# Kernel tuning notes

Hardware: AMD Instinct MI355X
Metric: run time of the kernel (lower is better)

## Reference

```python
import jax, jax.numpy as jnp
import numpy as np

N_WAY = 2
K_SHOT = 5
C = 320
NPTS = 2048
NQ = 2
K_PROTO = 100  # hardcoded k=100 in forward
N_CLS = N_WAY + 1
SIGMA = 1.0
NEG = -1e9


def _l2norm(x, eps=1e-8):
    return x / (jnp.linalg.norm(x, axis=-1, keepdims=True) + eps)


def _class_prototypes(feat, mask, k):
    """Multi-prototype masked pooling for one class.
    feat: [M, C] point features; mask: [M] float (1 = belongs to class).
    Picks k masked seed points, assigns every masked point to its
    nearest (cosine) seed, and returns the k masked cluster means.
    """
    M = feat.shape[0]
    # deterministic seeds: first k masked points (tie-break by index)
    score = mask - jnp.arange(M, dtype=feat.dtype) * 1e-9
    _, seed_idx = jax.lax.top_k(score, k)
    seeds = feat[seed_idx]                      # [k, C]
    sim = _l2norm(feat) @ _l2norm(seeds).T      # [M, k]
    assign = jnp.argmax(sim, axis=1)            # [M]
    onehot = jax.nn.one_hot(assign, k, dtype=feat.dtype) * mask[:, None]  # [M, k]
    num = onehot.T @ feat                       # [k, C]
    den = onehot.sum(axis=0)[:, None] + 1e-8
    return num / den


def _fg_prototypes(support_feat, fg_mask, k):
    # support_feat [n_way, k_shot, C, N] -> per-class point sets [n_way, k_shot*N, C]
    feat = support_feat.transpose(0, 1, 3, 2).reshape(N_WAY, -1, C)
    m = fg_mask.reshape(N_WAY, -1).astype(feat.dtype)
    protos = jax.vmap(lambda f, mm: _class_prototypes(f, mm, k))(feat, m)  # [n_way, k, C]
    labels = jnp.repeat(jnp.arange(1, N_WAY + 1), k)                        # classes 1..n_way
    return protos.reshape(-1, C), jax.nn.one_hot(labels, N_CLS, dtype=feat.dtype)


def _bg_prototypes(support_feat, bg_mask, k):
    feat = support_feat.transpose(0, 1, 3, 2).reshape(-1, C)   # all shots pooled
    m = bg_mask.reshape(-1).astype(feat.dtype)
    protos = _class_prototypes(feat, m, k)                      # [k, C]
    labels = jnp.zeros((k,), dtype=jnp.int32)                   # class 0 = background
    return protos, jax.nn.one_hot(labels, N_CLS, dtype=feat.dtype)


def _predict(prototypes, proto_onehot, qfeat, qlabels):
    # cosine similarity [M, P], per-class max over that class's prototypes
    sim = (_l2norm(qfeat) @ _l2norm(prototypes).T) / SIGMA        # [M, P]
    cls_mask = proto_onehot.T[None] > 0                            # [1, ncls, P]
    pred = jnp.max(jnp.where(cls_mask, sim[:, None, :], NEG), axis=-1)  # [M, ncls]
    logp = jax.nn.log_softmax(pred, axis=-1)
    loss = -jnp.mean(jnp.take_along_axis(logp, qlabels.reshape(-1, 1), axis=1))
    query_pred = pred.reshape(NQ, NPTS, N_CLS).transpose(0, 2, 1)  # [NQ, ncls, NPTS]
    return loss, query_pred


def reference(support_feat, query_feat, support_y, query_y):
    fg_mask = support_y
    bg_mask = 1 - support_y
    fg_protos, fg_labels = _fg_prototypes(support_feat, fg_mask, K_PROTO)
    bg_protos, bg_labels = _bg_prototypes(support_feat, bg_mask, K_PROTO)
    prototypes = jnp.concatenate([bg_protos, fg_protos], axis=0)           # [P, C]
    proto_labels = jnp.concatenate([bg_labels, fg_labels], axis=0)         # [P, ncls]

    qfeat = query_feat.transpose(0, 2, 1).reshape(-1, C)                   # [NQ*NPTS, C]
    loss, query_pred = _predict(prototypes, proto_labels, qfeat, query_y)
    # the forward adds computeCrossEntropyLoss(query_pred, query_y): same CE again
    loss = loss * 2.0

    # post-hoc per-point confidence thresholding (vectorized Python loop)
    qp = jnp.concatenate([query_pred[0], query_pred[1]], axis=-1)          # [ncls, NQ*NPTS]
    predictions = jnp.argmax(qp, axis=0)
    confidences = jnp.max(qp, axis=0)
    final = jnp.where(confidences > jnp.mean(confidences), predictions, -1)
    final_labels = jnp.stack([final[:NPTS], final[NPTS:]], axis=0)         # [2, NPTS]
    return loss, query_pred, final_labels


def setup_inputs() -> dict:
    key = jax.random.key(0)
    k1, k2, k3, k4 = jax.random.split(key, 4)
    return {
        "support_feat": jax.random.normal(k1, (N_WAY, K_SHOT, C, NPTS), dtype=jnp.float32),
        "query_feat": jax.random.normal(k2, (NQ, C, NPTS), dtype=jnp.float32),
        "support_y": jax.random.randint(k3, (N_WAY, K_SHOT, NPTS), 0, 2, dtype=jnp.int32),
        "query_y": jax.random.randint(k4, (NQ, NPTS), 0, 3, dtype=jnp.int32),
    }
```

## Files before the change

kernel.cpp:

```cpp
#include <hip/hip_runtime.h>
#include <math.h>

#define C 320
#define NPTS 2048
#define SUPPTS 20480
#define QPTS 4096
#define KP 100
#define NCLS 3
#define PSTRIDE 300

__global__ __launch_bounds__(64) void k_protoseed(const float* __restrict__ sup,
                                                  const int* __restrict__ sy,
                                                  float* __restrict__ pbP,
                                                  int* __restrict__ cntG) {
    int p    = blockIdx.x;
    int lane = threadIdx.x;
    if (lane == 0) cntG[p] = 0;
    int prob = (p < 100) ? 2 : ((p < 200) ? 0 : 1);
    int rank = (p < 100) ? p : ((p < 200) ? p - 100 : p - 200);
    int M    = (prob == 2) ? SUPPTS : 10240;
    int base = (prob == 1) ? 10240 : 0;
    int found = 0, sp = 0;
    for (int chunk = 0; chunk < M; chunk += 64) {
        int yy = sy[base + chunk + lane];
        int m  = (prob == 2) ? (1 - yy) : yy;
        unsigned long long bal = __ballot(m != 0);
        int cnt = __popcll(bal);
        if (found + cnt > rank) {
            int need = rank - found;
            int prefix = __popcll(bal & ((1ull << lane) - 1ull));
            unsigned long long match = __ballot(m && (prefix == need));
            int pos = __ffsll((unsigned long long)match) - 1;
            sp = base + chunk + pos;
            break;
        }
        found += cnt;
    }
    const float* fb = sup + ((size_t)(sp >> 11) * C) * NPTS + (sp & 2047);
    float v[5]; float s = 0.f;
    #pragma unroll
    for (int i = 0; i < 5; i++) {
        v[i] = fb[(size_t)(lane + i * 64) * NPTS];
        s += v[i] * v[i];
    }
    #pragma unroll
    for (int off = 32; off > 0; off >>= 1) s += __shfl_down(s, off);
    s = __shfl(s, 0);
    float r = 1.0f / (sqrtf(s) + 1e-8f);
    int tile, slot;
    if (p < 100)      { tile = p / 10;              slot = p % 10; }
    else if (p < 200) { tile = 10 + (p - 100) / 10; slot = (p - 100) % 10; }
    else              { tile = 20 + (p - 200) / 10; slot = (p - 200) % 10; }
    #pragma unroll
    for (int i = 0; i < 5; i++)
        pbP[(size_t)(lane + i * 64) * 480 + tile * 16 + slot] = v[i] * r;
}

__global__ __launch_bounds__(256) void k_assign(const float* __restrict__ sup,
                                                const float* __restrict__ pbP,
                                                float* __restrict__ pmaxv,
                                                int* __restrict__ pmaxj) {
    int b = blockIdx.x, jt = blockIdx.y, tid = threadIdx.x;
    int w = (b >= 40) ? 1 : 0;
    int g = b * 256 + tid;
    const float* fb = sup + ((size_t)(g >> 11) * C) * NPTS + (g & 2047);
    const float* rbb = pbP + (size_t)jt * 16;
    const float* rfb = pbP + (size_t)(10 + w * 10 + jt) * 16;
    float accB[10], accF[10];
    #pragma unroll
    for (int j = 0; j < 10; j++) { accB[j] = 0.f; accF[j] = 0.f; }
    float pf[8];
    #pragma unroll
    for (int k = 0; k < 8; k++) pf[k] = fb[(size_t)k * NPTS];
    for (int cc = 0; cc < C; cc += 8) {
        float cur[8];
        #pragma unroll
        for (int k = 0; k < 8; k++) cur[k] = pf[k];
        if (cc + 8 < C) {
            #pragma unroll
            for (int k = 0; k < 8; k++) pf[k] = fb[(size_t)(cc + 8 + k) * NPTS];
        }
        #pragma unroll
        for (int k = 0; k < 8; k++) {
            const float* rb = rbb + (size_t)(cc + k) * 480;
            const float* rf = rfb + (size_t)(cc + k) * 480;
            float px = cur[k];
            #pragma unroll
            for (int j = 0; j < 10; j++) {
                accB[j] += px * rb[j];
                accF[j] += px * rf[j];
            }
        }
    }
    float bvB = accB[0]; int bjB = 0;
    float bvF = accF[0]; int bjF = 0;
    #pragma unroll
    for (int j = 1; j < 10; j++) {
        if (accB[j] > bvB) { bvB = accB[j]; bjB = j; }
        if (accF[j] > bvF) { bvF = accF[j]; bjF = j; }
    }
    size_t a0 = (size_t)jt * 40960 + g;
    pmaxv[a0] = bvB;          pmaxj[a0] = jt * 10 + bjB;
    pmaxv[a0 + 20480] = bvF;  pmaxj[a0 + 20480] = jt * 10 + bjF;
}

__global__ __launch_bounds__(256) void k_combine_dst(const float* __restrict__ pmaxv,
                                                     const int* __restrict__ pmaxj,
                                                     const int* __restrict__ sy,
                                                     int* __restrict__ dst,
                                                     float* __restrict__ loss,
                                                     int* __restrict__ cntG) {
    int g = blockIdx.x * 256 + threadIdx.x;
    if (g == 0) loss[0] = 0.f;
    if (g == 1) loss[1] = 0.f;
    float bvB = pmaxv[g];         int bjB = pmaxj[g];
    float bvF = pmaxv[20480 + g]; int bjF = pmaxj[20480 + g];
    #pragma unroll
    for (int t = 1; t < 10; t++) {
        size_t base = (size_t)t * 40960;
        float vB = pmaxv[base + g];
        if (vB > bvB) { bvB = vB; bjB = pmaxj[base + g]; }
        float vF = pmaxv[base + 20480 + g];
        if (vF > bvF) { bvF = vF; bjF = pmaxj[base + 20480 + g]; }
    }
    int way = (g >= 10240) ? 1 : 0;
    int dv = sy[g] ? (100 + way * 100 + bjF) : bjB;
    dst[g] = dv;
    atomicAdd(&cntG[dv], 1);
}

__global__ __launch_bounds__(256) void k_accum_lds(const float* __restrict__ sup,
                                                   const int* __restrict__ dst,
                                                   float* __restrict__ part) {
    __shared__ float bins[4 * 200 * 16];
    __shared__ int   dl[1024];
    int bx = blockIdx.x;
    int by = blockIdx.y;
    int tid = threadIdx.x;
    int ws = bx >> 1, half = bx & 1;
    int wmask = (ws >= 5) ? 1 : 0;
    int c0 = by * 16;

    int4 d4 = *(const int4*)(dst + ws * 2048 + half * 1024 + 4 * tid);
    dl[4 * tid + 0] = (d4.x < 100) ? d4.x : (d4.x - wmask * 100);
    dl[4 * tid + 1] = (d4.y < 100) ? d4.y : (d4.y - wmask * 100);
    dl[4 * tid + 2] = (d4.z < 100) ? d4.z : (d4.z - wmask * 100);
    dl[4 * tid + 3] = (d4.w < 100) ? d4.w : (d4.w - wmask * 100);
    for (int i = tid; i < 4 * 200 * 16; i += 256) bins[i] = 0.f;
    __syncthreads();

    int wv = tid >> 6, lane = tid & 63;
    int ch = lane & 15, pq = lane >> 4;
    float* mybins = bins + wv * 3200;
    const int* dlp = dl + wv * 256 + pq;
    const float* fb = sup + ((size_t)(ws * C + c0 + ch)) * NPTS + half * 1024 + wv * 256 + pq;

    int   b_cur = dlp[0];
    float f_cur = fb[0];
    for (int it = 0; it < 64; it++) {
        int nidx = (it < 63) ? (it + 1) * 4 : 0;
        int   b_nxt = dlp[nidx];
        float f_nxt = fb[nidx];
        int b0 = __builtin_amdgcn_readlane(b_cur, 0);
        int b1 = __builtin_amdgcn_readlane(b_cur, 16);
        int b2 = __builtin_amdgcn_readlane(b_cur, 32);
        int b3 = __builtin_amdgcn_readlane(b_cur, 48);
        bool dup = (b0 == b1) | (b0 == b2) | (b0 == b3) |
                   (b1 == b2) | (b1 == b3) | (b2 == b3);
        int addr = b_cur * 16 + ch;
        if (!dup) {
            mybins[addr] += f_cur;
        } else {
            unsafeAtomicAdd(&mybins[addr], f_cur);
        }
        b_cur = b_nxt; f_cur = f_nxt;
    }
    __syncthreads();

    for (int i = tid; i < 3200; i += 256) {
        int bin = i >> 4, c = i & 15;
        float s = bins[bin * 16 + c] + bins[3200 + bin * 16 + c]
                + bins[6400 + bin * 16 + c] + bins[9600 + bin * 16 + c];
        int ct8 = by * 2 + (c >> 3);
        part[(size_t)(bx * 40 + ct8) * 1600 + bin * 8 + (c & 7)] = s;
    }
}

__global__ __launch_bounds__(64) void k_reduce_proto(const float* __restrict__ part,
                                                     const int* __restrict__ cntG,
                                                     float* __restrict__ phatT) {
    int d   = blockIdx.x;
    int tid = threadIdx.x;
    int local, s0, ns;
    if (d < 100)      { local = d;       s0 = 0;  ns = 20; }
    else if (d < 200) { local = d;       s0 = 0;  ns = 10; }
    else              { local = d - 100; s0 = 10; ns = 10; }
    float dn = (float)cntG[d];
    float inv = 1.0f / (dn + 1e-8f);
    float vals[5]; float sq = 0.f;
    #pragma unroll
    for (int i = 0; i < 5; i++) {
        int c = tid + i * 64;
        int ct = c >> 3, cl = c & 7;
        float s = 0.f;
        for (int k = 0; k < ns; k++)
            s += part[(size_t)((s0 + k) * 40 + ct) * 1600 + local * 8 + cl];
        float v = s * inv;
        vals[i] = v; sq += v * v;
    }
    #pragma unroll
    for (int off = 32; off > 0; off >>= 1) sq += __shfl_down(sq, off);
    sq = __shfl(sq, 0);
    float rn = 1.0f / (sqrtf(sq) + 1e-8f);
    #pragma unroll
    for (int i = 0; i < 5; i++)
        phatT[(size_t)(tid + i * 64) * PSTRIDE + d] = vals[i] * rn;
}

__global__ __launch_bounds__(256) void k_qpartial(const float* __restrict__ qry,
                                                  const float* __restrict__ phT,
                                                  float* __restrict__ qmaxv,
                                                  float* __restrict__ qrn) {
    __shared__ float shp[C * 16];
    __shared__ float red[3 * 64 * 45];
    int pb = blockIdx.x, jt = blockIdx.y, tid = threadIdx.x;
    int wave = tid >> 6, lane = tid & 63;
    int j0 = jt * 10;
    for (int i = tid; i < C * 10; i += 256) {
        int j = i % 10, c = i / 10;
        shp[c * 16 + j] = phT[(size_t)c * PSTRIDE + j0 + j];
    }
    __syncthreads();
    int m = pb * 256 + lane * 4;
    int c0 = wave * 80;
    const float* fb = qry + ((size_t)(m >> 11) * C + c0) * NPTS + (m & 2047);
    float acc[4][10];
    #pragma unroll
    for (int p = 0; p < 4; p++)
        #pragma unroll
        for (int j = 0; j < 10; j++) acc[p][j] = 0.f;
    float qn[4] = {0.f, 0.f, 0.f, 0.f};
    float4 pf[8];
    #pragma unroll
    for (int k = 0; k < 8; k++) pf[k] = *(const float4*)(fb + (size_t)k * NPTS);
    for (int cc = 0; cc < 80; cc += 8) {
        float4 cur[8];
        #pragma unroll
        for (int k = 0; k < 8; k++) cur[k] = pf[k];
        if (cc + 8 < 80) {
            #pragma unroll
            for (int k = 0; k < 8; k++) pf[k] = *(const float4*)(fb + (size_t)(cc + 8 + k) * NPTS);
        }
        #pragma unroll
        for (int k = 0; k < 8; k++) {
            const float* row = &shp[(c0 + cc + k) * 16];
            float4 p0 = ((const float4*)row)[0];
            float4 p1 = ((const float4*)row)[1];
            float2 p2 = ((const float2*)row)[4];
            float pr[10] = {p0.x,p0.y,p0.z,p0.w,p1.x,p1.y,p1.z,p1.w,p2.x,p2.y};
            float4 cv = cur[k];
            if (jt == 0) {
                qn[0] += cv.x*cv.x; qn[1] += cv.y*cv.y; qn[2] += cv.z*cv.z; qn[3] += cv.w*cv.w;
            }
            #pragma unroll
            for (int j = 0; j < 10; j++) {
                acc[0][j] += cv.x * pr[j];
                acc[1][j] += cv.y * pr[j];
                acc[2][j] += cv.z * pr[j];
                acc[3][j] += cv.w * pr[j];
            }
        }
    }
    if (wave > 0) {
        float* my = red + ((wave - 1) * 64 + lane) * 45;
        #pragma unroll
        for (int p = 0; p < 4; p++)
            #pragma unroll
            for (int j = 0; j < 10; j++) my[p * 10 + j] = acc[p][j];
        #pragma unroll
        for (int p = 0; p < 4; p++) my[40 + p] = qn[p];
    }
    __syncthreads();
    if (wave == 0) {
        #pragma unroll
        for (int w = 0; w < 3; w++) {
            const float* my = red + (w * 64 + lane) * 45;
            #pragma unroll
            for (int p = 0; p < 4; p++)
                #pragma unroll
                for (int j = 0; j < 10; j++) acc[p][j] += my[p * 10 + j];
            #pragma unroll
            for (int p = 0; p < 4; p++) qn[p] += my[40 + p];
        }
        #pragma unroll
        for (int p = 0; p < 4; p++) {
            float bv = acc[p][0];
            #pragma unroll
            for (int j = 1; j < 10; j++) bv = fmaxf(bv, acc[p][j]);
            qmaxv[(size_t)(m + p) * 30 + jt] = bv;
        }
        if (jt == 0) {
            #pragma unroll
            for (int p = 0; p < 4; p++) qrn[m + p] = 1.0f / (sqrtf(qn[p]) + 1e-8f);
        }
    }
}

__global__ __launch_bounds__(256) void k_pred(const float* __restrict__ qmaxv,
                                              const float* __restrict__ qrn,
                                              const int* __restrict__ qy,
                                              float* __restrict__ out,
                                              float* __restrict__ lossacc,
                                              float* __restrict__ cbuf,
                                              int* __restrict__ lbuf) {
    __shared__ float redL[256];
    __shared__ float redC[256];
    int tid = threadIdx.x;
    int m = blockIdx.x * 256 + tid;
    float rn = qrn[m];
    float pred[NCLS];
    #pragma unroll
    for (int cls = 0; cls < NCLS; cls++) {
        float g = qmaxv[(size_t)m * 30 + cls * 10];
        #pragma unroll
        for (int t = 1; t < 10; t++) g = fmaxf(g, qmaxv[(size_t)m * 30 + cls * 10 + t]);
        pred[cls] = rn * g;
    }
    int q = m >> 11, n = m & 2047;
    #pragma unroll
    for (int cls = 0; cls < NCLS; cls++)
        out[1 + ((size_t)(q * NCLS + cls)) * NPTS + n] = pred[cls];
    float mx = fmaxf(pred[0], fmaxf(pred[1], pred[2]));
    float lse = mx + logf(expf(pred[0] - mx) + expf(pred[1] - mx) + expf(pred[2] - mx));
    int lab = 0; float cf = pred[0];
    if (pred[1] > cf) { cf = pred[1]; lab = 1; }
    if (pred[2] > cf) { cf = pred[2]; lab = 2; }
    cbuf[m] = cf; lbuf[m] = lab;
    redL[tid] = lse - pred[qy[m]];
    redC[tid] = cf;
    __syncthreads();
    for (int off = 128; off > 0; off >>= 1) {
        if (tid < off) { redL[tid] += redL[tid + off]; redC[tid] += redC[tid + off]; }
        __syncthreads();
    }
    if (tid == 0) {
        atomicAdd(&lossacc[0], redL[0]);
        atomicAdd(&lossacc[1], redC[0]);
    }
}

__global__ __launch_bounds__(256) void k_final(const float* __restrict__ cbuf,
                                               const int* __restrict__ lbuf,
                                               const float* __restrict__ lossacc,
                                               float* __restrict__ out) {
    int m = blockIdx.x * 256 + threadIdx.x;
    float mean = lossacc[1] / (float)QPTS;
    float cf = cbuf[m];
    out[1 + 2 * NCLS * NPTS + m] = (cf > mean) ? (float)lbuf[m] : -1.0f;
    if (m == 0) out[0] = 2.0f * lossacc[0] / (float)QPTS;
}

extern "C" void kernel_launch(void* const* d_in, const int* in_sizes, int n_in,
                              void* d_out, int out_size, void* d_ws, size_t ws_size,
                              hipStream_t stream) {
    const float* sup = (const float*)d_in[0];
    const float* qry = (const float*)d_in[1];
    const int*   sy  = (const int*)d_in[2];
    const int*   qy  = (const int*)d_in[3];
    float* out = (float*)d_out;

    float* f      = (float*)d_ws;
    float* qrn    = f;
    float* cnt    = qrn + QPTS;
    int*   cntG   = (int*)cnt;
    float* pbufT  = cnt + 4000;
    float* phatT  = pbufT + 96000;
    float* loss   = phatT + 96000;
    int*   dstb   = (int*)(loss + 4);
    float* trans  = (float*)(dstb + SUPPTS);
    float* pmaxv  = trans;
    int*   pmaxj  = (int*)(pmaxv + 409600);
    float* pbP    = (float*)(pmaxj + 409600);
    float* part   = trans;
    float* qmaxv  = trans;
    float* cbuf   = qmaxv + 122880;
    int*   lbuf   = (int*)(cbuf + QPTS);

    k_protoseed<<<300, 64, 0, stream>>>(sup, sy, pbP, cntG);
    {
        dim3 grid(80, 10);
        k_assign<<<grid, 256, 0, stream>>>(sup, pbP, pmaxv, pmaxj);
    }
    k_combine_dst<<<80, 256, 0, stream>>>(pmaxv, pmaxj, sy, dstb, loss, cntG);
    {
        dim3 grid(20, 20);
        k_accum_lds<<<grid, 256, 0, stream>>>(sup, dstb, part);
    }
    k_reduce_proto<<<300, 64, 0, stream>>>(part, cntG, phatT);
    {
        dim3 grid(16, 30);
        k_qpartial<<<grid, 256, 0, stream>>>(qry, phatT, qmaxv, qrn);
    }
    k_pred<<<16, 256, 0, stream>>>(qmaxv, qrn, qy, out, loss, cbuf, lbuf);
    k_final<<<16, 256, 0, stream>>>(cbuf, lbuf, loss, out);
}
```

Measured before the change: 246.7 us.

## Stage assign prototypes in LDS and compute four points per thread with float4 loads

```diff
diff --git a/kernel.cpp b/kernel.cpp
--- a/kernel.cpp
+++ b/kernel.cpp
@@ -56,52 +56,76 @@
         pbP[(size_t)(lane + i * 64) * 480 + tile * 16 + slot] = v[i] * r;
 }
 
-__global__ __launch_bounds__(256) void k_assign(const float* __restrict__ sup,
+__global__ __launch_bounds__(128) void k_assign(const float* __restrict__ sup,
                                                 const float* __restrict__ pbP,
                                                 float* __restrict__ pmaxv,
                                                 int* __restrict__ pmaxj) {
+    __shared__ float shp[C * 24];
     int b = blockIdx.x, jt = blockIdx.y, tid = threadIdx.x;
-    int w = (b >= 40) ? 1 : 0;
-    int g = b * 256 + tid;
-    const float* fb = sup + ((size_t)(g >> 11) * C) * NPTS + (g & 2047);
-    const float* rbb = pbP + (size_t)jt * 16;
-    const float* rfb = pbP + (size_t)(10 + w * 10 + jt) * 16;
-    float accB[10], accF[10];
-    #pragma unroll
-    for (int j = 0; j < 10; j++) { accB[j] = 0.f; accF[j] = 0.f; }
-    float pf[8];
-    #pragma unroll
-    for (int k = 0; k < 8; k++) pf[k] = fb[(size_t)k * NPTS];
-    for (int cc = 0; cc < C; cc += 8) {
-        float cur[8];
-        #pragma unroll
-        for (int k = 0; k < 8; k++) cur[k] = pf[k];
-        if (cc + 8 < C) {
-            #pragma unroll
-            for (int k = 0; k < 8; k++) pf[k] = fb[(size_t)(cc + 8 + k) * NPTS];
-        }
-        #pragma unroll
-        for (int k = 0; k < 8; k++) {
-            const float* rb = rbb + (size_t)(cc + k) * 480;
-            const float* rf = rfb + (size_t)(cc + k) * 480;
-            float px = cur[k];
-            #pragma unroll
-            for (int j = 0; j < 10; j++) {
-                accB[j] += px * rb[j];
-                accF[j] += px * rf[j];
+    int w = (b >= 20) ? 1 : 0;
+    for (int i = tid; i < C * 10; i += 128) {
+        int c = i / 10, j = i % 10;
+        shp[c * 24 + j]      = pbP[(size_t)c * 480 + jt * 16 + j];
+        shp[c * 24 + 10 + j] = pbP[(size_t)c * 480 + (10 + w * 10 + jt) * 16 + j];
+    }
+    __syncthreads();
+    int g0 = b * 512 + 4 * tid;
+    const float* fb = sup + ((size_t)(g0 >> 11) * C) * NPTS + (g0 & 2047);
+    float accB[4][10], accF[4][10];
+    #pragma unroll
+    for (int p = 0; p < 4; p++)
+        #pragma unroll
+        for (int j = 0; j < 10; j++) { accB[p][j] = 0.f; accF[p][j] = 0.f; }
+    float4 pf[4];
+    #pragma unroll
+    for (int k = 0; k < 4; k++) pf[k] = *(const float4*)(fb + (size_t)k * NPTS);
+    for (int cc = 0; cc < C; cc += 4) {
+        float4 cur[4];
+        #pragma unroll
+        for (int k = 0; k < 4; k++) cur[k] = pf[k];
+        if (cc + 4 < C) {
+            #pragma unroll
+            for (int k = 0; k < 4; k++) pf[k] = *(const float4*)(fb + (size_t)(cc + 4 + k) * NPTS);
+        }
+        #pragma unroll
+        for (int k = 0; k < 4; k++) {
+            const float4* row = (const float4*)&shp[(cc + k) * 24];
+            float4 r0 = row[0], r1 = row[1], r2 = row[2], r3 = row[3], r4 = row[4];
+            float px[4] = {cur[k].x, cur[k].y, cur[k].z, cur[k].w};
+            #pragma unroll
+            for (int p = 0; p < 4; p++) {
+                float x = px[p];
+                accB[p][0] += x * r0.x; accB[p][1] += x * r0.y;
+                accB[p][2] += x * r0.z; accB[p][3] += x * r0.w;
+                accB[p][4] += x * r1.x; accB[p][5] += x * r1.y;
+                accB[p][6] += x * r1.z; accB[p][7] += x * r1.w;
+                accB[p][8] += x * r2.x; accB[p][9] += x * r2.y;
+                accF[p][0] += x * r2.z; accF[p][1] += x * r2.w;
+                accF[p][2] += x * r3.x; accF[p][3] += x * r3.y;
+                accF[p][4] += x * r3.z; accF[p][5] += x * r3.w;
+                accF[p][6] += x * r4.x; accF[p][7] += x * r4.y;
+                accF[p][8] += x * r4.z; accF[p][9] += x * r4.w;
             }
         }
     }
-    float bvB = accB[0]; int bjB = 0;
-    float bvF = accF[0]; int bjF = 0;
-    #pragma unroll
-    for (int j = 1; j < 10; j++) {
-        if (accB[j] > bvB) { bvB = accB[j]; bjB = j; }
-        if (accF[j] > bvF) { bvF = accF[j]; bjF = j; }
-    }
-    size_t a0 = (size_t)jt * 40960 + g;
-    pmaxv[a0] = bvB;          pmaxj[a0] = jt * 10 + bjB;
-    pmaxv[a0 + 20480] = bvF;  pmaxj[a0 + 20480] = jt * 10 + bjF;
+    float bvB[4], bvF[4]; int bjB[4], bjF[4];
+    #pragma unroll
+    for (int p = 0; p < 4; p++) {
+        bvB[p] = accB[p][0]; bjB[p] = 0;
+        bvF[p] = accF[p][0]; bjF[p] = 0;
+        #pragma unroll
+        for (int j = 1; j < 10; j++) {
+            if (accB[p][j] > bvB[p]) { bvB[p] = accB[p][j]; bjB[p] = j; }
+            if (accF[p][j] > bvF[p]) { bvF[p] = accF[p][j]; bjF[p] = j; }
+        }
+    }
+    size_t a0 = (size_t)jt * 40960 + g0;
+    *(float4*)(pmaxv + a0) = make_float4(bvB[0], bvB[1], bvB[2], bvB[3]);
+    *(int4*)(pmaxj + a0) = make_int4(jt * 10 + bjB[0], jt * 10 + bjB[1],
+                                     jt * 10 + bjB[2], jt * 10 + bjB[3]);
+    *(float4*)(pmaxv + a0 + 20480) = make_float4(bvF[0], bvF[1], bvF[2], bvF[3]);
+    *(int4*)(pmaxj + a0 + 20480) = make_int4(jt * 10 + bjF[0], jt * 10 + bjF[1],
+                                             jt * 10 + bjF[2], jt * 10 + bjF[3]);
 }
 
 __global__ __launch_bounds__(256) void k_combine_dst(const float* __restrict__ pmaxv,
@@ -388,8 +412,8 @@
 
     k_protoseed<<<300, 64, 0, stream>>>(sup, sy, pbP, cntG);
     {
-        dim3 grid(80, 10);
-        k_assign<<<grid, 256, 0, stream>>>(sup, pbP, pmaxv, pmaxj);
+        dim3 grid(40, 10);
+        k_assign<<<grid, 128, 0, stream>>>(sup, pbP, pmaxv, pmaxj);
     }
     k_combine_dst<<<80, 256, 0, stream>>>(pmaxv, pmaxj, sy, dstb, loss, cntG);
     {
```

New measurement: 259.6 us. 1.05x slower.
